# Performance work log

Hardware: AMD Instinct MI355X
Metric: run time of the kernel (lower is better)

## Reference

```python
import jax, jax.numpy as jnp
import numpy as np

N, E, IN_DIM, H, D = 100000, 1600000, 128, 4, 32


def setup_inputs() -> dict:
    key = jax.random.key(0)
    ks = jax.random.split(key, 8)
    glorot = lambda k, shape: jax.random.uniform(
        k, shape, jnp.float32, -1.0, 1.0) * np.sqrt(6.0 / (shape[0] + shape[1]))
    return {
        "x": jax.random.normal(ks[0], (N, IN_DIM), jnp.float32),
        "row": jax.random.randint(ks[1], (E,), 0, N, jnp.int32),
        "col": jax.random.randint(ks[2], (E,), 0, N, jnp.int32),
        "W_l": glorot(ks[3], (IN_DIM, H * D)),
        "W_r": glorot(ks[4], (IN_DIM, H * D)),
        "a1w": glorot(ks[5], (IN_DIM, H)),
        "a2w": glorot(ks[6], (IN_DIM, H)),
        "bias": jnp.zeros((H * D,), jnp.float32),
    }


def reference(x, row, col, W_l, W_r, a1w, a2w, bias):
    n = x.shape[0]  # num_nodes (= graph[0].max()+1 with dense random rows)
    x_l = (x @ W_l).reshape(n, H, D)          # [N,H,D]
    x_r = x @ W_r                              # [N,H*D]
    # per-edge attention logits: a1[row] + a2[col], leaky-relu(0.2)
    attn = jax.nn.leaky_relu((x @ a1w)[row] + (x @ a2w)[col], 0.2)  # [E,H]
    # segment softmax over destination rows (numerically stable)
    m = jax.ops.segment_max(attn, row, num_segments=n)               # [N,H]
    e = jnp.exp(attn - m[row])
    s = jax.ops.segment_sum(e, row, num_segments=n)                  # [N,H]
    attn_d = e / s[row]                                              # [E,H]
    # per-head SpMM: scatter-add weighted source features to destinations
    msgs = attn_d[:, :, None] * x_l[col]                             # [E,H,D]
    out = jax.ops.segment_sum(msgs, row, num_segments=n).reshape(n, H * D)
    return out + x_r + bias
```

## Files before the change

### kernel.cpp

```cpp
#include <hip/hip_runtime.h>


typedef short bfvec8 __attribute__((ext_vector_type(8)));
typedef float f32x4  __attribute__((ext_vector_type(4)));

#define BK 256
#define CAP 6144
#define EPB 4096
#define REC 272

__device__ __forceinline__ unsigned short f2bf(float f) {
  union { float f; unsigned int i; } v; v.f = f;
  unsigned int r = v.i + 0x7fffu + ((v.i >> 16) & 1u);
  return (unsigned short)(r >> 16);
}

__global__ __launch_bounds__(128) void wprep_k(
    const float* __restrict__ Wl, const float* __restrict__ Wr,
    const float* __restrict__ a1w, const float* __restrict__ a2w,
    unsigned short* __restrict__ Wtg)
{
  const int n = blockIdx.x;
  const int y = blockIdx.y;
  const int k = threadIdx.x;
  const float* W = y ? Wr : Wl;
  const float* A = y ? a2w : a1w;
  const float LOG2E = 1.4426950408889634f;
  float v = (n < 128) ? W[(size_t)k * 128 + n] : A[k * 4 + (n - 128)] * LOG2E;
  Wtg[((size_t)y * 132 + n) * 128 + k] = f2bf(v);
}

__global__ __launch_bounds__(256) void gemm_mfma(
    const float* __restrict__ x, const unsigned short* __restrict__ Wtg,
    const float* __restrict__ bias,
    char* __restrict__ xls, float* __restrict__ out,
    float* __restrict__ s1, int N)
{
  __shared__ unsigned short xs[64][136];
  __shared__ unsigned short Ws[132][136];
  const int t = threadIdx.x;
  const int n0 = blockIdx.x * 64;

  for (int i = t; i < 2048; i += 256) {
    int rr = i >> 5, kc = (i & 31) << 2;
    float4 v = make_float4(0.f, 0.f, 0.f, 0.f);
    int n = n0 + rr;
    if (n < N) v = *(const float4*)&x[(size_t)n * 128 + kc];
    unsigned int lo = (unsigned int)f2bf(v.x) | ((unsigned int)f2bf(v.y) << 16);
    unsigned int hi = (unsigned int)f2bf(v.z) | ((unsigned int)f2bf(v.w) << 16);
    *(uint2*)&xs[rr][kc] = make_uint2(lo, hi);
  }

  const int w    = t >> 6;
  const int lane = t & 63;
  const int m    = lane & 15;
  const int quad = lane >> 4;

  #pragma unroll
  for (int y = 0; y < 2; ++y) {
    const unsigned short* Wt = Wtg + (size_t)y * 132 * 128;
    if (y) __syncthreads();
    for (int i = t; i < 2112; i += 256) {
      int nr = i >> 4, kc = (i & 15) << 3;
      *(uint4*)&Ws[nr][kc] = *(const uint4*)&Wt[(size_t)nr * 128 + kc];
    }
    __syncthreads();

    f32x4 acc[9];
    #pragma unroll
    for (int i = 0; i < 9; ++i) acc[i] = (f32x4){0.f, 0.f, 0.f, 0.f};

    #pragma unroll
    for (int kc = 0; kc < 128; kc += 32) {
      bfvec8 af = *(const bfvec8*)&xs[16 * w + m][kc + quad * 8];
      #pragma unroll
      for (int nt = 0; nt < 9; ++nt) {
        int nr = nt * 16 + m; if (nr > 131) nr = 131;
        bfvec8 bfr = *(const bfvec8*)&Ws[nr][kc + quad * 8];
        acc[nt] = __builtin_amdgcn_mfma_f32_16x16x32_bf16(af, bfr, acc[nt], 0, 0, 0);
      }
    }

    #pragma unroll
    for (int nt = 0; nt < 8; ++nt) {
      int c = nt * 16 + m;
      float b = y ? bias[c] : 0.f;
      #pragma unroll
      for (int r = 0; r < 4; ++r) {
        int n = n0 + 16 * w + quad * 4 + r;
        if (n < N) {
          float v = acc[nt][r] + b;
          if (y) out[(size_t)n * 128 + c] = v;
          else   *(unsigned short*)(xls + (size_t)n * REC + 2 * c) = f2bf(v);
        }
      }
    }
    if (m < 4) {
      #pragma unroll
      for (int r = 0; r < 4; ++r) {
        int n = n0 + 16 * w + quad * 4 + r;
        if (n < N) {
          if (y) *(float*)(xls + (size_t)n * REC + 256 + 4 * m) = acc[8][r];
          else   s1[n * 4 + m] = acc[8][r];
        }
      }
    }
  }
}

__global__ __launch_bounds__(512) void init_k(int* __restrict__ bcur, int NBK) {
  int b = threadIdx.x;
  if (b < NBK) bcur[b] = b * CAP;
}

__global__ __launch_bounds__(256) void bin_k(const int* __restrict__ row,
    const int* __restrict__ col, int* __restrict__ bcur,
    unsigned int* __restrict__ binned, int E, int NBK)
{
  __shared__ int h[512];
  __shared__ int base[512];
  const int t = threadIdx.x;
  const int e0 = blockIdx.x * EPB;
  const int e1 = min(e0 + EPB, E);

  int rloc[16];
  for (int i = t; i < NBK; i += 256) h[i] = 0;
  __syncthreads();
  #pragma unroll
  for (int k = 0; k < 16; ++k) {
    int e = e0 + t + (k << 8);
    rloc[k] = (e < e1) ? row[e] : -1;
    if (rloc[k] >= 0) atomicAdd(&h[rloc[k] >> 8], 1);
  }
  __syncthreads();
  for (int i = t; i < NBK; i += 256) {
    int c = h[i];
    base[i] = c ? atomicAdd(&bcur[i], c) : 0;
  }
  __syncthreads();
  for (int i = t; i < NBK; i += 256) h[i] = 0;
  __syncthreads();
  #pragma unroll
  for (int k = 0; k < 16; ++k) {
    int e = e0 + t + (k << 8);
    if (e < e1) {
      int r = rloc[k];
      unsigned c = (unsigned)col[e];
      int b = r >> 8;
      int rk = atomicAdd(&h[b], 1);
      binned[base[b] + rk] = ((unsigned)(r & 255) << 17) | c;
    }
  }
}

__global__ __launch_bounds__(256) void csr_k(const unsigned int* __restrict__ binned,
    const int* __restrict__ bcur, int* __restrict__ offs, int* __restrict__ deg,
    unsigned int* __restrict__ colsort, int N)
{
  __shared__ int h[BK];
  __shared__ int sh[BK];
  const int t = threadIdx.x;
  const int b = blockIdx.x;
  const int lo = b * BK;
  const int e0 = b * CAP;
  const int e1 = bcur[b];

  h[t] = 0;
  __syncthreads();
  for (int i = e0 + t; i < e1; i += 256)
    atomicAdd(&h[binned[i] >> 17], 1);
  __syncthreads();

  int v = h[t];
  sh[t] = v;
  __syncthreads();
  for (int off = 1; off < 256; off <<= 1) {
    int tv = (t >= off) ? sh[t - off] : 0;
    __syncthreads();
    sh[t] += tv;
    __syncthreads();
  }
  int ex = sh[t] - v;
  int node = lo + t;
  if (node < N) { offs[node] = e0 + ex; deg[node] = v; }

  h[t] = ex;
  __syncthreads();
  for (int i = e0 + t; i < e1; i += 256) {
    unsigned p = binned[i];
    int rlo = p >> 17;
    unsigned c = p & 0x1FFFFu;
    int pos = atomicAdd(&h[rlo], 1);
    colsort[e0 + pos] = c * REC;
  }
}

__global__ __launch_bounds__(256) void agg_k(const int* __restrict__ offs,
    const int* __restrict__ deg, const unsigned int* __restrict__ colsort,
    const float* __restrict__ s1, const char* __restrict__ xls,
    float* __restrict__ out, int N)
{
  const int lane = threadIdx.x & 63;
  const int n = blockIdx.x * 4 + (threadIdx.x >> 6);
  if (n >= N) return;
  const int e0 = offs[n], e1 = e0 + deg[n];
  const int h  = lane >> 4;
  const int hp = lane & 3;
  const int jj = (lane >> 2) & 7;
  const float s1h = s1[n * 4 + h];
  const float s1c = s1[n * 4 + hp];
  const unsigned lane4 = (unsigned)(lane << 2);
  const unsigned h256  = 256u + (unsigned)(h << 2);
  const unsigned hp256 = 256u + (unsigned)(hp << 2);

  float acc0 = 0.f, acc1 = 0.f, wsum = 0.f;
  int i0 = e0;
  for (; i0 + 8 <= e1; i0 += 8) {
    unsigned csl = colsort[i0 + jj];
    float z2 = *(const float*)(xls + (csl + hp256));
    float z = s1c + z2;
    z = fmaxf(z, 0.2f * z);
    float wv = exp2f(z);

    unsigned cs[8];
    #pragma unroll
    for (int j = 0; j < 8; ++j) cs[j] = colsort[i0 + j];
    unsigned pv[8];
    #pragma unroll
    for (int j = 0; j < 8; ++j)
      pv[j] = *(const unsigned*)(xls + (cs[j] + lane4));

    #pragma unroll
    for (int j = 0; j < 8; ++j) {
      float wj = __shfl(wv, (j << 2) | h);
      wsum += wj;
      union { unsigned u; float f; } lo, hi;
      lo.u = pv[j] << 16;
      hi.u = pv[j] & 0xffff0000u;
      acc0 += wj * lo.f;
      acc1 += wj * hi.f;
    }
  }
  for (; i0 < e1; ++i0) {
    unsigned cs = colsort[i0];
    float z2 = *(const float*)(xls + (cs + h256));
    unsigned p = *(const unsigned*)(xls + (cs + lane4));
    float z = s1h + z2;
    z = fmaxf(z, 0.2f * z);
    float wv = exp2f(z);
    wsum += wv;
    union { unsigned u; float f; } lo, hi;
    lo.u = p << 16; hi.u = p & 0xffff0000u;
    acc0 += wv * lo.f;
    acc1 += wv * hi.f;
  }

  float inv = (wsum > 0.f) ? (1.0f / wsum) : 0.f;
  const size_t o = (size_t)n * 128 + 2 * lane;
  float2 xr = *(const float2*)&out[o];
  float2 res; res.x = acc0 * inv + xr.x; res.y = acc1 * inv + xr.y;
  *(float2*)&out[o] = res;
}

extern "C" void kernel_launch(void* const* d_in, const int* in_sizes, int n_in,
                              void* d_out, int out_size, void* d_ws, size_t ws_size,
                              hipStream_t stream) {
  const float* x    = (const float*)d_in[0];
  const int*   row  = (const int*)d_in[1];
  const int*   col  = (const int*)d_in[2];
  const float* Wl   = (const float*)d_in[3];
  const float* Wr   = (const float*)d_in[4];
  const float* a1w  = (const float*)d_in[5];
  const float* a2w  = (const float*)d_in[6];
  const float* bias = (const float*)d_in[7];
  float* out = (float*)d_out;
  const int N = in_sizes[0] / 128;
  const int E = in_sizes[1];
  (void)n_in; (void)out_size; (void)ws_size;

  const int NBK = (N + BK - 1) / BK;

  char* ws = (char*)d_ws;
  size_t off = 0;
  auto carve = [&](size_t bytes) { void* p = ws + off; off += (bytes + 255) & ~(size_t)255; return p; };
  char* xls            = (char*)carve((size_t)N * REC);
  float* s1            = (float*)carve((size_t)N * 4 * 4);
  int* offs            = (int*)carve((size_t)N * 4);
  int* deg             = (int*)carve((size_t)N * 4);
  unsigned int* colsort= (unsigned int*)carve((size_t)NBK * CAP * 4);
  unsigned int* binned = (unsigned int*)carve((size_t)NBK * CAP * 4);
  int* bcur            = (int*)carve((size_t)NBK * 4);
  unsigned short* Wtg  = (unsigned short*)carve((size_t)2 * 132 * 128 * 2);

  wprep_k  <<<dim3(132, 2), 128, 0, stream>>>(Wl, Wr, a1w, a2w, Wtg);
  gemm_mfma<<<(N + 63) / 64, 256, 0, stream>>>(x, Wtg, bias, xls, out, s1, N);
  init_k   <<<1, 512, 0, stream>>>(bcur, NBK);
  bin_k    <<<(E + EPB - 1) / EPB, 256, 0, stream>>>(row, col, bcur, binned, E, NBK);
  csr_k    <<<NBK, 256, 0, stream>>>(binned, bcur, offs, deg, colsort, N);
  agg_k    <<<(N + 3) / 4, 256, 0, stream>>>(offs, deg, colsort, s1, xls, out, N);
}
```

Baseline: 302.5 us.

## Split attention logits out of feature records and batch the edge tail

The per-node a2 logit is moved out of the 272-byte feature record into its own dense s2 array, so feature records are 256 bytes and aligned, and each source row is addressed with a shift. The aggregation reads the logit from the compact s2 array (colsort>>4 indexing), which should cut cache lines touched per edge. The scalar remainder loop is replaced by one masked 8-wide batch that reuses the shuffle-based weight path, so leftover edges issue their gathers in parallel. In exchange it adds an extra workspace array and redundant clamped loads for padded tail lanes.

```diff
diff --git a/kernel.cpp b/kernel.cpp
--- a/kernel.cpp
+++ b/kernel.cpp
@@ -7,7 +7,7 @@
 #define BK 256
 #define CAP 6144
 #define EPB 4096
-#define REC 272
+#define REC 256
 
 __device__ __forceinline__ unsigned short f2bf(float f) {
   union { float f; unsigned int i; } v; v.f = f;
@@ -34,7 +34,7 @@
     const float* __restrict__ x, const unsigned short* __restrict__ Wtg,
     const float* __restrict__ bias,
     char* __restrict__ xls, float* __restrict__ out,
-    float* __restrict__ s1, int N)
+    float* __restrict__ s1, float* __restrict__ s2, int N)
 {
   __shared__ unsigned short xs[64][136];
   __shared__ unsigned short Ws[132][136];
@@ -91,7 +91,7 @@
         if (n < N) {
           float v = acc[nt][r] + b;
           if (y) out[(size_t)n * 128 + c] = v;
-          else   *(unsigned short*)(xls + (size_t)n * REC + 2 * c) = f2bf(v);
+          else   *(unsigned short*)(xls + ((size_t)n << 8) + 2 * c) = f2bf(v);
         }
       }
     }
@@ -100,7 +100,7 @@
       for (int r = 0; r < 4; ++r) {
         int n = n0 + 16 * w + quad * 4 + r;
         if (n < N) {
-          if (y) *(float*)(xls + (size_t)n * REC + 256 + 4 * m) = acc[8][r];
+          if (y) s2[n * 4 + m] = acc[8][r];
           else   s1[n * 4 + m] = acc[8][r];
         }
       }
@@ -191,14 +191,14 @@
     int rlo = p >> 17;
     unsigned c = p & 0x1FFFFu;
     int pos = atomicAdd(&h[rlo], 1);
-    colsort[e0 + pos] = c * REC;
+    colsort[e0 + pos] = c << 8;
   }
 }
 
 __global__ __launch_bounds__(256) void agg_k(const int* __restrict__ offs,
     const int* __restrict__ deg, const unsigned int* __restrict__ colsort,
-    const float* __restrict__ s1, const char* __restrict__ xls,
-    float* __restrict__ out, int N)
+    const float* __restrict__ s1, const float* __restrict__ s2,
+    const char* __restrict__ xls, float* __restrict__ out, int N)
 {
   const int lane = threadIdx.x & 63;
   const int n = blockIdx.x * 4 + (threadIdx.x >> 6);
@@ -207,17 +207,16 @@
   const int h  = lane >> 4;
   const int hp = lane & 3;
   const int jj = (lane >> 2) & 7;
-  const float s1h = s1[n * 4 + h];
   const float s1c = s1[n * 4 + hp];
   const unsigned lane4 = (unsigned)(lane << 2);
-  const unsigned h256  = 256u + (unsigned)(h << 2);
-  const unsigned hp256 = 256u + (unsigned)(hp << 2);
+  const unsigned hp4   = (unsigned)(hp << 2);
+  const char* s2b = (const char*)s2;
 
   float acc0 = 0.f, acc1 = 0.f, wsum = 0.f;
   int i0 = e0;
   for (; i0 + 8 <= e1; i0 += 8) {
     unsigned csl = colsort[i0 + jj];
-    float z2 = *(const float*)(xls + (csl + hp256));
+    float z2 = *(const float*)(s2b + ((csl >> 4) + hp4));
     float z = s1c + z2;
     z = fmaxf(z, 0.2f * z);
     float wv = exp2f(z);
@@ -241,18 +240,32 @@
       acc1 += wj * hi.f;
     }
   }
-  for (; i0 < e1; ++i0) {
-    unsigned cs = colsort[i0];
-    float z2 = *(const float*)(xls + (cs + h256));
-    unsigned p = *(const unsigned*)(xls + (cs + lane4));
-    float z = s1h + z2;
+  if (i0 < e1) {
+    const int rem = e1 - i0;
+    unsigned csl = colsort[i0 + (jj < rem ? jj : rem - 1)];
+    float z2 = *(const float*)(s2b + ((csl >> 4) + hp4));
+    float z = s1c + z2;
     z = fmaxf(z, 0.2f * z);
-    float wv = exp2f(z);
-    wsum += wv;
-    union { unsigned u; float f; } lo, hi;
-    lo.u = p << 16; hi.u = p & 0xffff0000u;
-    acc0 += wv * lo.f;
-    acc1 += wv * hi.f;
+    float wv = (jj < rem) ? exp2f(z) : 0.f;
+
+    unsigned cs[8];
+    #pragma unroll
+    for (int j = 0; j < 8; ++j) cs[j] = colsort[i0 + (j < rem ? j : rem - 1)];
+    unsigned pv[8];
+    #pragma unroll
+    for (int j = 0; j < 8; ++j)
+      pv[j] = *(const unsigned*)(xls + (cs[j] + lane4));
+
+    #pragma unroll
+    for (int j = 0; j < 8; ++j) {
+      float wj = __shfl(wv, (j << 2) | h);
+      wsum += wj;
+      union { unsigned u; float f; } lo, hi;
+      lo.u = pv[j] << 16;
+      hi.u = pv[j] & 0xffff0000u;
+      acc0 += wj * lo.f;
+      acc1 += wj * hi.f;
+    }
   }
 
   float inv = (wsum > 0.f) ? (1.0f / wsum) : 0.f;
@@ -285,6 +298,7 @@
   auto carve = [&](size_t bytes) { void* p = ws + off; off += (bytes + 255) & ~(size_t)255; return p; };
   char* xls            = (char*)carve((size_t)N * REC);
   float* s1            = (float*)carve((size_t)N * 4 * 4);
+  float* s2            = (float*)carve((size_t)N * 4 * 4);
   int* offs            = (int*)carve((size_t)N * 4);
   int* deg             = (int*)carve((size_t)N * 4);
   unsigned int* colsort= (unsigned int*)carve((size_t)NBK * CAP * 4);
@@ -293,9 +307,9 @@
   unsigned short* Wtg  = (unsigned short*)carve((size_t)2 * 132 * 128 * 2);
 
   wprep_k  <<<dim3(132, 2), 128, 0, stream>>>(Wl, Wr, a1w, a2w, Wtg);
-  gemm_mfma<<<(N + 63) / 64, 256, 0, stream>>>(x, Wtg, bias, xls, out, s1, N);
+  gemm_mfma<<<(N + 63) / 64, 256, 0, stream>>>(x, Wtg, bias, xls, out, s1, s2, N);
   init_k   <<<1, 512, 0, stream>>>(bcur, NBK);
   bin_k    <<<(E + EPB - 1) / EPB, 256, 0, stream>>>(row, col, bcur, binned, E, NBK);
   csr_k    <<<NBK, 256, 0, stream>>>(binned, bcur, offs, deg, colsort, N);
-  agg_k    <<<(N + 3) / 4, 256, 0, stream>>>(offs, deg, colsort, s1, xls, out, N);
-}
+  agg_k    <<<(N + 3) / 4, 256, 0, stream>>>(offs, deg, colsort, s1, s2, xls, out, N);
+}
```

After: 285.4 us. 1.06x faster.
